# Optimization experiments

Hardware: AMD Instinct MI355X
Metric: run time of the kernel (lower is better)

Reference implementation:

```python
import jax, jax.numpy as jnp
import numpy as np

D_K = 64


def setup_inputs() -> dict:
    key = jax.random.key(0)
    ks = jax.random.split(key, 5)
    B, S, D, H, DK, DV = 4, 2048, 1024, 16, 64, 64
    # xavier_normal-ish scale for the per-head projections
    std_qk = (2.0 / (D + DK)) ** 0.5
    std_o = (2.0 / (H * DV + D)) ** 0.5
    return {
        "x": jax.random.normal(ks[0], (B, S, D), dtype=jnp.float32),
        "W_Q": jax.random.normal(ks[1], (H, D, DK), dtype=jnp.float32) * std_qk,
        "W_K": jax.random.normal(ks[2], (H, D, DK), dtype=jnp.float32) * std_qk,
        "W_V": jax.random.normal(ks[3], (H, D, DV), dtype=jnp.float32) * std_qk,
        "W_O": jax.random.normal(ks[4], (H * DV, D), dtype=jnp.float32) * std_o,
    }


def reference(x, W_Q, W_K, W_V, W_O):
    # x: [B,S,D]; W_Q/W_K: [H,D,dk]; W_V: [H,D,dv]; W_O: [H*dv, D]
    q = jnp.einsum("bsd,hdk->bhsk", x, W_Q)
    k = jnp.einsum("bsd,hdk->bhsk", x, W_K)
    v = jnp.einsum("bsd,hdv->bhsv", x, W_V)
    scale = 1.0 / jnp.sqrt(jnp.asarray(D_K, dtype=x.dtype))
    scores = jnp.einsum("bhsk,bhtk->bhst", q, k) * scale  # [B,H,S,S]
    attn = jax.nn.softmax(scores, axis=-1)
    out = jnp.einsum("bhst,bhtv->bhsv", attn, v)  # [B,H,S,dv]
    B, H, S, DV = out.shape
    # concat heads along feature dim: head i occupies [i*dv:(i+1)*dv]
    out = jnp.transpose(out, (0, 2, 1, 3)).reshape(B, S, H * DV)
    return out @ W_O  # [B,S,D]
```

## Files before the change

### kernel.cpp

```cpp
#include <hip/hip_runtime.h>
#include <hip/hip_bf16.h>
#include <cstdint>
#include <cstddef>


typedef __attribute__((ext_vector_type(8))) __bf16 bf16v8;
typedef __attribute__((ext_vector_type(4))) float f32x4;
typedef __attribute__((ext_vector_type(16))) float f32x16;
typedef __attribute__((ext_vector_type(8))) unsigned short u16x8;
typedef __attribute__((ext_vector_type(4))) unsigned u32x4;
typedef unsigned short ushort_t;

#define AS3(p) ((__attribute__((address_space(3))) void*)(p))
#define AS1C(p) ((const __attribute__((address_space(1))) void*)(p))

__device__ __forceinline__ ushort_t f2bf(float f) {
  unsigned u = __builtin_bit_cast(unsigned, f);
  unsigned r = u + 0x7FFFu + ((u >> 16) & 1u);
  return (ushort_t)(r >> 16);
}

__device__ __forceinline__ unsigned cvt_pk_bf16(float lo, float hi) {
  unsigned r;
  asm("v_cvt_pk_bf16_f32 %0, %1, %2" : "=v"(r) : "v"(lo), "v"(hi));
  return r;
}

__device__ __forceinline__ void plswap(unsigned& x, unsigned& y) {
  asm("v_permlane32_swap_b32 %0, %1" : "+v"(x), "+v"(y));
}

__device__ __forceinline__ float exp2_raw(float x) {
  float r;
  asm("v_exp_f32 %0, %1" : "=v"(r) : "v"(x));
  return r;
}

constexpr int B_ = 4, S_ = 2048, D_ = 1024, H_ = 16, DK_ = 64;
constexpr int M_ = B_ * S_;
constexpr int NQKV_ = 3 * H_ * DK_;
constexpr float QSCALE = 0.125f * 1.44269504088896f;

__global__ __launch_bounds__(256) void cast_x_kernel(const float* __restrict__ x,
                                                     ushort_t* __restrict__ xb) {
  size_t i = (size_t)blockIdx.x * 256 + threadIdx.x;
  const float4* px = (const float4*)(x + i * 8);
  float4 a = px[0], b = px[1];
  u16x8 v;
  v[0] = f2bf(a.x); v[1] = f2bf(a.y); v[2] = f2bf(a.z); v[3] = f2bf(a.w);
  v[4] = f2bf(b.x); v[5] = f2bf(b.y); v[6] = f2bf(b.z); v[7] = f2bf(b.w);
  size_t di = i ^ ((i >> 8) & 3);
  *(u16x8*)(xb + di * 8) = v;
}

__global__ __launch_bounds__(256) void prep_wqkv_kernel(const float* __restrict__ Wq,
                                                        const float* __restrict__ Wk,
                                                        const float* __restrict__ Wv,
                                                        ushort_t* __restrict__ dst) {
  int idx = blockIdx.x * 256 + threadIdx.x;
  int p = idx >> 20;
  int rem = idx & 0xFFFFF;
  int h = rem >> 16;
  int dk = (rem >> 10) & 63;
  int d = rem & 1023;
  const float* W = (p == 0) ? Wq : ((p == 1) ? Wk : Wv);
  float v = W[(h << 16) + (d << 6) + dk];
  if (p == 0) v *= QSCALE;
  dst[idx ^ (((idx >> 11) & 3) << 3)] = f2bf(v);
}

__global__ __launch_bounds__(256) void prep_wo_kernel(const float* __restrict__ Wo,
                                                      ushort_t* __restrict__ dst) {
  int idx = blockIdx.x * 256 + threadIdx.x;
  int n = idx >> 10, k = idx & 1023;
  dst[idx] = f2bf(Wo[(k << 10) + n]);
}

#define VMW(N) asm volatile("s_waitcnt vmcnt(" N ")" ::: "memory")
#define BAR() asm volatile("s_barrier" ::: "memory")

#define STAGE3(T)                                                                   \
  {                                                                                 \
    const int pb = (((T) + 3) & 3) * 32768;                                         \
    __builtin_amdgcn_global_load_lds(AS1C(gA0), AS3(lds + pb + wid * 1024), 16, 0, 0); \
    __builtin_amdgcn_global_load_lds(AS1C(gA1), AS3(lds + pb + 8192 + wid * 1024), 16, 0, 0); \
    __builtin_amdgcn_global_load_lds(AS1C(gB0), AS3(lds + pb + 16384 + wid * 1024), 16, 0, 0); \
    __builtin_amdgcn_global_load_lds(AS1C(gB1), AS3(lds + pb + 24576 + wid * 1024), 16, 0, 0); \
    gA0 += 32; gA1 += 32; gB0 += 32; gB1 += 32;                                     \
  }

#define TILE_BODY(T, VMSTR, DO_STAGE)                                               \
  {                                                                                 \
    const int cb = ((T) & 3) * 32768;                                               \
    VMW(VMSTR);                                                                     \
    BAR();                                                                          \
    if (DO_STAGE) STAGE3(T);                                                        \
    bf16v8 af[8], bfr[4];                                                           \
    _Pragma("unroll")                                                               \
    for (int i = 0; i < 8; ++i)                                                     \
      af[i] = *(const bf16v8*)(lds + cb + awo + i * 1024);                          \
    _Pragma("unroll")                                                               \
    for (int j = 0; j < 4; ++j)                                                     \
      bfr[j] = *(const bf16v8*)(lds + cb + bwo + j * 1024);                         \
    __builtin_amdgcn_s_setprio(1);                                                  \
    _Pragma("unroll")                                                               \
    for (int i = 0; i < 8; ++i)                                                     \
      _Pragma("unroll")                                                             \
      for (int j = 0; j < 4; ++j)                                                   \
        acc[i][j] = __builtin_amdgcn_mfma_f32_16x16x32_bf16(af[i], bfr[j], acc[i][j], 0, 0, 0); \
    __builtin_amdgcn_s_setprio(0);                                                  \
  }

__global__ __launch_bounds__(512) void gemm256_qkv(
    const ushort_t* __restrict__ A, const ushort_t* __restrict__ Bt,
    ushort_t* __restrict__ qb, ushort_t* __restrict__ kb, ushort_t* __restrict__ vt) {
  extern __shared__ __align__(16) char lds[];
  const int tid = threadIdx.x;
  const int wid = tid >> 6, lane = tid & 63;
  const int g = lane >> 4, lq = lane & 15;
  const int wm = wid >> 2, wn = wid & 3;
  const int bid = blockIdx.x;
  const int wg = (bid & 7) * 48 + (bid >> 3);
  const int mb = wg / 12, nb = wg % 12;
  const int m0 = mb * 256, n0 = nb * 256;

  const int co = (g ^ ((lq >> 1) & 3)) * 16;
  const int awo = wm * 8192 + lq * 64 + co;
  const int bwo = 16384 + wn * 4096 + lq * 64 + co;

  const ushort_t* gA0 = A + (size_t)(m0 + (tid >> 2)) * 1024 + (tid & 3) * 8;
  const ushort_t* gA1 = gA0 + (size_t)128 * 1024;
  const ushort_t* gB0 = Bt + (size_t)(n0 + (tid >> 2)) * 1024 + (tid & 3) * 8;
  const ushort_t* gB1 = gB0 + (size_t)128 * 1024;

  f32x4 acc[8][4] = {};

  STAGE3(-3); STAGE3(-2); STAGE3(-1);

  for (int t = 0; t < 28; ++t) TILE_BODY(t, "8", true);
  TILE_BODY(28, "8", true);
  TILE_BODY(29, "8", false);
  TILE_BODY(30, "4", false);
  TILE_BODY(31, "0", false);

  asm volatile("s_waitcnt lgkmcnt(0)" ::: "memory");
  BAR();
  const int p = n0 >> 10;
  if (p == 2) {
#pragma unroll
    for (int i = 0; i < 8; ++i)
#pragma unroll
      for (int j = 0; j < 4; ++j) {
        int col = wn * 64 + j * 16 + lq;
        int swz = (col & 7) << 4;
#pragma unroll
        for (int r = 0; r < 4; ++r) {
          int row = wm * 128 + i * 16 + g * 4 + r;
          *(ushort_t*)(lds + ((col * 512 + row * 2) ^ swz)) = f2bf(acc[i][j][r]);
        }
      }
  } else {
#pragma unroll
    for (int i = 0; i < 8; ++i)
#pragma unroll
      for (int j = 0; j < 4; ++j) {
        int col = wn * 64 + j * 16 + lq;
#pragma unroll
        for (int r = 0; r < 4; ++r) {
          int row = wm * 128 + i * 16 + g * 4 + r;
          *(ushort_t*)(lds + ((row * 512 + col * 2) ^ ((row & 7) << 4))) = f2bf(acc[i][j][r]);
        }
      }
  }
  asm volatile("s_waitcnt lgkmcnt(0)" ::: "memory");
  BAR();

  if (p == 0) {
#pragma unroll
    for (int it = 0; it < 16; ++it) {
      int ci = it * 512 + tid;
      int row = ci >> 5, ch = ci & 31;
      u16x8 v = *(const u16x8*)(lds + ((row * 512 + ch * 16) ^ ((row & 7) << 4)));
      int gcol = n0 + ch * 8;
      int h = (gcol >> 6) & 15, dd0 = gcol & 63;
      int grow = m0 + row;
      int b = grow >> 11, s = grow & 2047;
      size_t bh = (size_t)(b * 16 + h);
      *(u16x8*)(qb + (bh * 2048 + s) * 64 + dd0) = v;
    }
  } else if (p == 1) {
#pragma unroll
    for (int it = 0; it < 16; ++it) {
      int ci = it * 512 + tid;
      int row = ci >> 5, ch = ci & 31;
      u16x8 v = *(const u16x8*)(lds + ((row * 512 + ch * 16) ^ ((row & 7) << 4)));
      int gcol = n0 + ch * 8;
      int h = (gcol >> 6) & 15, dd0 = gcol & 63;
      int grow = m0 + row;
      int b = grow >> 11, s = grow & 2047;
      size_t bh = (size_t)(b * 16 + h);
      int tt = s >> 6, sIn = s & 63;
      int byte = (sIn * 128 + dd0 * 2) ^ ((sIn & 7) << 4);
      *(u16x8*)((char*)kb + (((size_t)bh * 32 + tt) << 13) + byte) = v;
    }
  } else {
#pragma unroll
    for (int it = 0; it < 16; ++it) {
      int ci = it * 512 + tid;
      int crow = ci >> 5, ch = ci & 31;
      u16x8 v = *(const u16x8*)(lds + ((crow * 512 + ch * 16) ^ ((crow & 7) << 4)));
      int gcol = n0 + crow;
      int h = (gcol >> 6) & 15, dd = gcol & 63;
      int grow = m0 + ch * 8;
      int b = grow >> 11, s = grow & 2047;
      size_t bh = (size_t)(b * 16 + h);
      int tt = s >> 6, sIn0 = s & 63;
      int byte = (dd * 128 + sIn0 * 2) ^ ((dd & 7) << 4);
      *(u16x8*)((char*)vt + (((size_t)bh * 32 + tt) << 13) + byte) = v;
    }
  }
}

__global__ __launch_bounds__(256) void gemm_bt(
    const ushort_t* __restrict__ A, const ushort_t* __restrict__ Bt,
    int NB, int K, float* __restrict__ Cf, int Ncols) {
  __shared__ ushort_t Al[128 * 32];
  __shared__ ushort_t Bl[128 * 32];
  const int tid = threadIdx.x;
  const int wid = tid >> 6, lane = tid & 63;
  const int g = lane >> 4, lq = lane & 15;
  const int mb = blockIdx.x / NB, nb = blockIdx.x % NB;
  const int m0 = mb * 128, n0 = nb * 128;
  const int wm = wid >> 1, wn = wid & 1;
  f32x4 acc[4][4] = {};
  const int c0 = wid * 128 + lane;

  for (int k0 = 0; k0 < K; k0 += 32) {
#pragma unroll
    for (int i = 0; i < 2; ++i) {
      int c = c0 + i * 64;
      int row = c >> 2, col = (c & 3) << 3;
      __builtin_amdgcn_global_load_lds(AS1C(A + (size_t)(m0 + row) * K + k0 + col),
                                       AS3(Al + (wid * 2 + i) * 512), 16, 0, 0);
      __builtin_amdgcn_global_load_lds(AS1C(Bt + (size_t)(n0 + row) * K + k0 + col),
                                       AS3(Bl + (wid * 2 + i) * 512), 16, 0, 0);
    }
    __syncthreads();
    bf16v8 af[4], bfr[4];
#pragma unroll
    for (int t = 0; t < 4; ++t)
      af[t] = *(const bf16v8*)&Al[(wm * 64 + t * 16 + lq) * 32 + g * 8];
#pragma unroll
    for (int t = 0; t < 4; ++t)
      bfr[t] = *(const bf16v8*)&Bl[(wn * 64 + t * 16 + lq) * 32 + g * 8];
#pragma unroll
    for (int i = 0; i < 4; ++i)
#pragma unroll
      for (int j = 0; j < 4; ++j)
        acc[i][j] = __builtin_amdgcn_mfma_f32_16x16x32_bf16(af[i], bfr[j], acc[i][j], 0, 0, 0);
    __syncthreads();
  }

#pragma unroll
  for (int i = 0; i < 4; ++i)
#pragma unroll
    for (int j = 0; j < 4; ++j)
#pragma unroll
      for (int r = 0; r < 4; ++r) {
        int row = m0 + wm * 64 + i * 16 + g * 4 + r;
        int col = n0 + wn * 64 + j * 16 + lq;
        Cf[(size_t)row * Ncols + col] = acc[i][j][r];
      }
}

__device__ __forceinline__ void softpack(const f32x16& s0, const f32x16& s1,
                                         float& lsum, bf16v8& pa0, bf16v8& pa1,
                                         bf16v8& pa2, bf16v8& pa3) {
  float e0[16], e1[16];
#pragma unroll
  for (int r = 0; r < 16; ++r) e0[r] = exp2_raw(s0[r]);
#pragma unroll
  for (int r = 0; r < 16; ++r) e1[r] = exp2_raw(s1[r]);
  float ad[16];
#pragma unroll
  for (int r = 0; r < 16; ++r) ad[r] = e0[r] + e1[r];
#pragma unroll
  for (int st = 8; st >= 1; st >>= 1)
#pragma unroll
    for (int r = 0; r < st; ++r) ad[r] += ad[r + st];
  lsum += ad[0];
  unsigned a0 = cvt_pk_bf16(e0[0], e0[1]), b0 = cvt_pk_bf16(e0[4], e0[5]);
  unsigned a1 = cvt_pk_bf16(e0[2], e0[3]), b1 = cvt_pk_bf16(e0[6], e0[7]);
  unsigned a2 = cvt_pk_bf16(e0[8], e0[9]), b2 = cvt_pk_bf16(e0[12], e0[13]);
  unsigned a3 = cvt_pk_bf16(e0[10], e0[11]), b3 = cvt_pk_bf16(e0[14], e0[15]);
  unsigned a4 = cvt_pk_bf16(e1[0], e1[1]), b4 = cvt_pk_bf16(e1[4], e1[5]);
  unsigned a5 = cvt_pk_bf16(e1[2], e1[3]), b5 = cvt_pk_bf16(e1[6], e1[7]);
  unsigned a6 = cvt_pk_bf16(e1[8], e1[9]), b6 = cvt_pk_bf16(e1[12], e1[13]);
  unsigned a7 = cvt_pk_bf16(e1[10], e1[11]), b7 = cvt_pk_bf16(e1[14], e1[15]);
  plswap(a0, b0); plswap(a1, b1); plswap(a2, b2); plswap(a3, b3);
  plswap(a4, b4); plswap(a5, b5); plswap(a6, b6); plswap(a7, b7);
  pa0 = __builtin_bit_cast(bf16v8, u32x4{a0, a1, b0, b1});
  pa1 = __builtin_bit_cast(bf16v8, u32x4{a2, a3, b2, b3});
  pa2 = __builtin_bit_cast(bf16v8, u32x4{a4, a5, b4, b5});
  pa3 = __builtin_bit_cast(bf16v8, u32x4{a6, a7, b6, b7});
}

#define MFMA32(a, b, c) __builtin_amdgcn_mfma_f32_32x32x16_bf16(a, b, c, 0, 0, 0)

#define ASTAGE(T)                                                                   \
  {                                                                                 \
    const int pb = ((T) & 1) * 16384;                                               \
    const char* ks = kbase + ((size_t)(T) << 13);                                   \
    const char* vs = vbase + ((size_t)(T) << 13);                                   \
    _Pragma("unroll")                                                               \
    for (int j = 0; j < 2; ++j) {                                                   \
      __builtin_amdgcn_global_load_lds(AS1C(ks + w * 2048 + j * 1024 + lane * 16),  \
                                       AS3(smem + pb + w * 2048 + j * 1024), 16, 0, 0); \
      __builtin_amdgcn_global_load_lds(AS1C(vs + w * 2048 + j * 1024 + lane * 16),  \
                                       AS3(smem + pb + 8192 + w * 2048 + j * 1024), 16, 0, 0); \
    }                                                                               \
  }

#define ACOMPUTE(T)                                                                 \
  {                                                                                 \
    const char* bk = smem + ((T) & 1) * 16384;                                      \
    bf16v8 kf0[4], kf1[4], vfr[2][4];                                               \
    _Pragma("unroll")                                                               \
    for (int c = 0; c < 4; ++c) {                                                   \
      kf0[c] = *(const bf16v8*)(bk + addr4[c]);                                     \
      kf1[c] = *(const bf16v8*)(bk + addr4[c] + 4096);                              \
    }                                                                               \
    _Pragma("unroll")                                                               \
    for (int nb = 0; nb < 2; ++nb)                                                  \
      _Pragma("unroll")                                                             \
      for (int ks2 = 0; ks2 < 4; ++ks2)                                             \
        vfr[nb][ks2] = *(const bf16v8*)(bk + addr4[ks2] + 8192 + nb * 4096);        \
    f32x16 s0 = {}, s1 = {};                                                        \
    __builtin_amdgcn_s_setprio(1);                                                  \
    _Pragma("unroll")                                                               \
    for (int c = 0; c < 4; ++c) {                                                   \
      s0 = MFMA32(kf0[c], qf[c], s0);                                               \
      s1 = MFMA32(kf1[c], qf[c], s1);                                               \
    }                                                                               \
    __builtin_amdgcn_s_setprio(0);                                                  \
    bf16v8 pa0, pa1, pa2, pa3;                                                      \
    softpack(s0, s1, lsum, pa0, pa1, pa2, pa3);                                     \
    __builtin_amdgcn_s_setprio(1);                                                  \
    _Pragma("unroll")                                                               \
    for (int nb = 0; nb < 2; ++nb) {                                                \
      oa[nb] = MFMA32(pa0, vfr[nb][0], oa[nb]);                                     \
      oa[nb] = MFMA32(pa1, vfr[nb][1], oa[nb]);                                     \
      oa[nb] = MFMA32(pa2, vfr[nb][2], oa[nb]);                                     \
      oa[nb] = MFMA32(pa3, vfr[nb][3], oa[nb]);                                     \
    }                                                                               \
    __builtin_amdgcn_s_setprio(0);                                                  \
  }

__global__ __launch_bounds__(256) void attn_kernel(const ushort_t* __restrict__ qb,
                                                   const ushort_t* __restrict__ kt,
                                                   const ushort_t* __restrict__ vt,
                                                   ushort_t* __restrict__ aout) {
  __shared__ __align__(16) char smem[32768];
  __shared__ float cbuf[4][32];
  const int tid = threadIdx.x;
  const int w = tid >> 6, lane = tid & 63;
  const int hi = lane >> 5, l31 = lane & 31;
  const int bidx = blockIdx.x;
  const int xcd = bidx & 7, slot = bidx >> 3;
  const int bh = xcd + 8 * (slot >> 4);
  const int qt = (slot & 15) * 4 + w;
  const char* kbase = (const char*)kt + ((size_t)bh << 18);
  const char* vbase = (const char*)vt + ((size_t)bh << 18);
  const ushort_t* Qp = qb + (size_t)bh * (S_ * 64) + qt * 32 * 64;

  bf16v8 qf[4];
#pragma unroll
  for (int c = 0; c < 4; ++c)
    qf[c] = *(const bf16v8*)(Qp + l31 * 64 + c * 16 + hi * 8);

  int addr4[4];
#pragma unroll
  for (int c = 0; c < 4; ++c)
    addr4[c] = (l31 * 128 + c * 32 + hi * 16) ^ ((l31 & 7) << 4);

  f32x16 oa[2] = {};
  float lsum = 0.f;

  ASTAGE(0);

#pragma unroll 2
  for (int t = 0; t < 31; ++t) {
    BAR();
    ASTAGE(t + 1);
    VMW("4");
    BAR();
    ACOMPUTE(t);
  }
  BAR();
  VMW("0");
  BAR();
  ACOMPUTE(31);

  lsum += __shfl_xor(lsum, 32);
  ushort_t* ob = (ushort_t*)(smem + w * 4096);
  cbuf[w][l31] = 1.0f / lsum;
  asm volatile("s_waitcnt lgkmcnt(0)" ::: "memory");
#pragma unroll
  for (int rq = 0; rq < 4; ++rq) {
    f32x4 c4 = *(const f32x4*)&cbuf[w][8 * rq + 4 * hi];
#pragma unroll
    for (int j = 0; j < 4; ++j) {
      int row = 8 * rq + 4 * hi + j;
#pragma unroll
      for (int nb = 0; nb < 2; ++nb)
        ob[row * 64 + nb * 32 + l31] = f2bf(oa[nb][4 * rq + j] * c4[j]);
    }
  }
  asm volatile("s_waitcnt lgkmcnt(0)" ::: "memory");
  const int row = lane >> 1, hf = lane & 1;
  const int b = bh >> 4, h = bh & 15;
  size_t obase = ((size_t)(b * S_ + qt * 32 + row)) * 1024 + h * 64 + hf * 32;
#pragma unroll
  for (int i = 0; i < 4; ++i) {
    bf16v8 v = *(const bf16v8*)&ob[row * 64 + hf * 32 + i * 8];
    *(bf16v8*)(aout + obase + i * 8) = v;
  }
}

extern "C" void kernel_launch(void* const* d_in, const int* in_sizes, int n_in,
                              void* d_out, int out_size, void* d_ws, size_t ws_size,
                              hipStream_t stream) {
  const float* x = (const float*)d_in[0];
  const float* Wq = (const float*)d_in[1];
  const float* Wk = (const float*)d_in[2];
  const float* Wv = (const float*)d_in[3];
  const float* Wo = (const float*)d_in[4];
  float* out = (float*)d_out;

  char* ws = (char*)d_ws;
  constexpr size_t OFF_XB = 0;
  constexpr size_t OFF_WQKV = 16777216;
  constexpr size_t OFF_WO = 23068672;
  constexpr size_t OFF_Q = 25165824;
  constexpr size_t OFF_K = 41943040;
  constexpr size_t OFF_V = 58720256;
  constexpr size_t OFF_AO = 75497472;
  constexpr size_t WS_NEEDED = 92274688;
  if (ws_size < WS_NEEDED) return;

  ushort_t* xb = (ushort_t*)(ws + OFF_XB);
  ushort_t* wqkv_t = (ushort_t*)(ws + OFF_WQKV);
  ushort_t* wo_t = (ushort_t*)(ws + OFF_WO);
  ushort_t* q_buf = (ushort_t*)(ws + OFF_Q);
  ushort_t* k_t = (ushort_t*)(ws + OFF_K);
  ushort_t* v_t = (ushort_t*)(ws + OFF_V);
  ushort_t* a_out = (ushort_t*)(ws + OFF_AO);

  cast_x_kernel<<<(M_ * D_ / 8) / 256, 256, 0, stream>>>(x, xb);
  prep_wqkv_kernel<<<(3 * H_ * DK_ * D_) / 256, 256, 0, stream>>>(Wq, Wk, Wv, wqkv_t);
  prep_wo_kernel<<<(D_ * D_) / 256, 256, 0, stream>>>(Wo, wo_t);

  gemm256_qkv<<<(M_ / 256) * (NQKV_ / 256), 512, 131072, stream>>>(
      xb, wqkv_t, q_buf, k_t, v_t);

  attn_kernel<<<1024, 256, 0, stream>>>(q_buf, k_t, v_t, a_out);

  gemm_bt<<<(M_ / 128) * (D_ / 128), 256, 0, stream>>>(
      a_out, wo_t, D_ / 128, D_, out, D_);
}
```

Measured before the change: 218.2 us.

## Replace output projection GEMM with 4-stage pipelined 256x128 swizzled kernel

Replaces the simple output-projection GEMM, which synchronised twice per K step, with a 512-thread 256x128-tile kernel. It uses a 4-deep async global-to-LDS prefetch pipeline with vmcnt waits, a single barrier per K step, MFMA priority boosting and block-index remapping for L2 locality. To avoid LDS bank conflicts, the attention output and the transposed W_O are written with an XOR chunk swizzle that the new kernel's fragment reads undo. The cost is more LDS per block (96KB), which limits occupancy, and the GEMM is now hard-coded to these dimensions.

```diff
diff --git a/kernel.cpp b/kernel.cpp
--- a/kernel.cpp
+++ b/kernel.cpp
@@ -73,7 +73,7 @@
                                                       ushort_t* __restrict__ dst) {
   int idx = blockIdx.x * 256 + threadIdx.x;
   int n = idx >> 10, k = idx & 1023;
-  dst[idx] = f2bf(Wo[(k << 10) + n]);
+  dst[idx ^ (((idx >> 11) & 3) << 3)] = f2bf(Wo[(k << 10) + n]);
 }
 
 #define VMW(N) asm volatile("s_waitcnt vmcnt(" N ")" ::: "memory")
@@ -221,55 +221,76 @@
   }
 }
 
-__global__ __launch_bounds__(256) void gemm_bt(
+#define OSTAGE(T)                                                                   \
+  {                                                                                 \
+    const int pb = ((T) & 3) * 24576;                                               \
+    __builtin_amdgcn_global_load_lds(AS1C(gA0), AS3(lds + pb + wid * 2048), 16, 0, 0); \
+    __builtin_amdgcn_global_load_lds(AS1C(gA1), AS3(lds + pb + wid * 2048 + 1024), 16, 0, 0); \
+    __builtin_amdgcn_global_load_lds(AS1C(gB0), AS3(lds + pb + 16384 + wid * 1024), 16, 0, 0); \
+    gA0 += 32; gA1 += 32; gB0 += 32;                                                \
+  }
+
+#define OBODY(T, VMSTR, DO_STAGE)                                                   \
+  {                                                                                 \
+    const int cb = ((T) & 3) * 24576;                                               \
+    VMW(VMSTR);                                                                     \
+    BAR();                                                                          \
+    if (DO_STAGE) OSTAGE((T) + 3);                                                  \
+    bf16v8 af[8], bfr[2];                                                           \
+    _Pragma("unroll")                                                               \
+    for (int i = 0; i < 8; ++i)                                                     \
+      af[i] = *(const bf16v8*)(lds + cb + awo + i * 1024);                          \
+    _Pragma("unroll")                                                               \
+    for (int j = 0; j < 2; ++j)                                                     \
+      bfr[j] = *(const bf16v8*)(lds + cb + bwo + j * 1024);                         \
+    __builtin_amdgcn_s_setprio(1);                                                  \
+    _Pragma("unroll")                                                               \
+    for (int i = 0; i < 8; ++i)                                                     \
+      _Pragma("unroll")                                                             \
+      for (int j = 0; j < 2; ++j)                                                   \
+        acc[i][j] = __builtin_amdgcn_mfma_f32_16x16x32_bf16(af[i], bfr[j], acc[i][j], 0, 0, 0); \
+    __builtin_amdgcn_s_setprio(0);                                                  \
+  }
+
+__global__ __launch_bounds__(512) void gemm256_op(
     const ushort_t* __restrict__ A, const ushort_t* __restrict__ Bt,
-    int NB, int K, float* __restrict__ Cf, int Ncols) {
-  __shared__ ushort_t Al[128 * 32];
-  __shared__ ushort_t Bl[128 * 32];
+    float* __restrict__ Cf) {
+  extern __shared__ __align__(16) char lds[];
   const int tid = threadIdx.x;
   const int wid = tid >> 6, lane = tid & 63;
   const int g = lane >> 4, lq = lane & 15;
-  const int mb = blockIdx.x / NB, nb = blockIdx.x % NB;
-  const int m0 = mb * 128, n0 = nb * 128;
-  const int wm = wid >> 1, wn = wid & 1;
-  f32x4 acc[4][4] = {};
-  const int c0 = wid * 128 + lane;
-
-  for (int k0 = 0; k0 < K; k0 += 32) {
-#pragma unroll
-    for (int i = 0; i < 2; ++i) {
-      int c = c0 + i * 64;
-      int row = c >> 2, col = (c & 3) << 3;
-      __builtin_amdgcn_global_load_lds(AS1C(A + (size_t)(m0 + row) * K + k0 + col),
-                                       AS3(Al + (wid * 2 + i) * 512), 16, 0, 0);
-      __builtin_amdgcn_global_load_lds(AS1C(Bt + (size_t)(n0 + row) * K + k0 + col),
-                                       AS3(Bl + (wid * 2 + i) * 512), 16, 0, 0);
-    }
-    __syncthreads();
-    bf16v8 af[4], bfr[4];
-#pragma unroll
-    for (int t = 0; t < 4; ++t)
-      af[t] = *(const bf16v8*)&Al[(wm * 64 + t * 16 + lq) * 32 + g * 8];
-#pragma unroll
-    for (int t = 0; t < 4; ++t)
-      bfr[t] = *(const bf16v8*)&Bl[(wn * 64 + t * 16 + lq) * 32 + g * 8];
-#pragma unroll
-    for (int i = 0; i < 4; ++i)
-#pragma unroll
-      for (int j = 0; j < 4; ++j)
-        acc[i][j] = __builtin_amdgcn_mfma_f32_16x16x32_bf16(af[i], bfr[j], acc[i][j], 0, 0, 0);
-    __syncthreads();
-  }
-
-#pragma unroll
-  for (int i = 0; i < 4; ++i)
-#pragma unroll
-    for (int j = 0; j < 4; ++j)
+  const int wm = wid >> 2, wn = wid & 3;
+  const int bid = blockIdx.x;
+  const int wg = (bid & 7) * 32 + (bid >> 3);
+  const int mb = wg >> 3, nb = wg & 7;
+  const int m0 = mb * 256, n0 = nb * 128;
+
+  const int co = (g ^ ((lq >> 1) & 3)) * 16;
+  const int awo = wm * 8192 + lq * 64 + co;
+  const int bwo = 16384 + wn * 2048 + lq * 64 + co;
+
+  const ushort_t* gA0 = A + (size_t)(m0 + wid * 32 + (lane >> 2)) * 1024 + (lane & 3) * 8;
+  const ushort_t* gA1 = gA0 + (size_t)16 * 1024;
+  const ushort_t* gB0 = Bt + (size_t)(n0 + wid * 16 + (lane >> 2)) * 1024 + (lane & 3) * 8;
+
+  f32x4 acc[8][2] = {};
+
+  OSTAGE(0); OSTAGE(1); OSTAGE(2);
+
+  for (int t = 0; t < 29; ++t) OBODY(t, "6", true);
+  OBODY(29, "6", false);
+  OBODY(30, "3", false);
+  OBODY(31, "0", false);
+
+#pragma unroll
+  for (int i = 0; i < 8; ++i)
+#pragma unroll
+    for (int j = 0; j < 2; ++j)
 #pragma unroll
       for (int r = 0; r < 4; ++r) {
-        int row = m0 + wm * 64 + i * 16 + g * 4 + r;
-        int col = n0 + wn * 64 + j * 16 + lq;
-        Cf[(size_t)row * Ncols + col] = acc[i][j][r];
+        int row = m0 + wm * 128 + i * 16 + g * 4 + r;
+        int col = n0 + wn * 32 + j * 16 + lq;
+        Cf[(size_t)row * 1024 + col] = acc[i][j][r];
       }
 }
 
@@ -419,11 +440,14 @@
   asm volatile("s_waitcnt lgkmcnt(0)" ::: "memory");
   const int row = lane >> 1, hf = lane & 1;
   const int b = bh >> 4, h = bh & 15;
-  size_t obase = ((size_t)(b * S_ + qt * 32 + row)) * 1024 + h * 64 + hf * 32;
+  const int rowg = b * 2048 + qt * 32 + row;
+  const int sx = (rowg >> 1) & 3;
+  size_t rbase = (size_t)rowg * 1024;
 #pragma unroll
   for (int i = 0; i < 4; ++i) {
     bf16v8 v = *(const bf16v8*)&ob[row * 64 + hf * 32 + i * 8];
-    *(bf16v8*)(aout + obase + i * 8) = v;
+    int c = h * 8 + hf * 4 + i;
+    *(bf16v8*)(aout + rbase + (size_t)((c ^ sx) * 8)) = v;
   }
 }
 
@@ -465,6 +489,5 @@
 
   attn_kernel<<<1024, 256, 0, stream>>>(q_buf, k_t, v_t, a_out);
 
-  gemm_bt<<<(M_ / 128) * (D_ / 128), 256, 0, stream>>>(
-      a_out, wo_t, D_ / 128, D_, out, D_);
-}
+  gemm256_op<<<(M_ / 256) * (D_ / 128), 512, 98304, stream>>>(a_out, wo_t, out);
+}
```

Result: faster. 208.5 us (-4.5%).
